# Performance work log

Measured on AMD Instinct MI355X. Metric: run time of the kernel, lower is better.

The kernel has to match this reference:

```python
import jax, jax.numpy as jnp
import numpy as np

TOPK = 2
EPS = 1e-6  # RMSNorm epsilon


def setup_inputs() -> dict:
    key = jax.random.key(0)
    ks = jax.random.split(key, 8)
    b, t, d, h, n = 2, 1024, 1024, 2048, 16
    x = jax.random.normal(ks[0], (b, t, d), dtype=jnp.float32)
    router_w = jax.random.normal(ks[1], (n, d), dtype=jnp.float32) * (1.0 / np.sqrt(d))
    router_bias = jnp.zeros((n,), dtype=jnp.float32)
    bank_mag = jax.random.normal(ks[2], (n, d, h), dtype=jnp.float32) * (1.0 / np.sqrt(d))
    bank_freq = jax.random.uniform(ks[3], (n, d, h), dtype=jnp.float32, minval=0.5, maxval=2.0) * (1.0 / np.sqrt(d))
    bank_phase = jax.random.uniform(ks[4], (n, h), dtype=jnp.float32, minval=-0.3, maxval=0.3)
    bank_down = jax.random.normal(ks[5], (n, h, d), dtype=jnp.float32) * (1.0 / np.sqrt(h))
    norm_w = jnp.ones((d,), dtype=jnp.float32)
    return {
        'x': x, 'router_w': router_w, 'router_bias': router_bias,
        'bank_mag': bank_mag, 'bank_freq': bank_freq, 'bank_phase': bank_phase,
        'bank_down': bank_down, 'norm_w': norm_w,
    }


def reference(x, router_w, router_bias, bank_mag, bank_freq, bank_phase, bank_down, norm_w):
    b, t, d = x.shape
    # Router: scores [b,t,n], top-k selection, softmax over selected logits
    scores = jnp.einsum('btd,nd->btn', x, router_w) + router_bias
    topv, topi = jax.lax.top_k(scores, TOPK)            # [b,t,k]
    weights = jax.nn.softmax(topv, axis=-1)             # [b,t,k]

    fx = x.reshape(b * t, d)                            # [T,d]
    # Dense per-expert compute (mathematically identical to per-token gather+bmm):
    mag = jnp.einsum('td,ndh->tnh', fx, bank_mag)       # [T,n,h]
    freq = jnp.einsum('td,ndh->tnh', fx, bank_freq)     # [T,n,h]
    hidden = jnp.tanh(mag) * jnp.cos(jax.nn.softplus(freq) + 0.1 + bank_phase[None, :, :])
    out_all = jnp.einsum('tnh,nhd->tnd', hidden, bank_down)  # [T,n,d]

    # Gather the top-k expert outputs per token and combine with routing weights
    ti = topi.reshape(b * t, TOPK)                      # [T,k]
    sel = jnp.take_along_axis(out_all, ti[:, :, None], axis=1)  # [T,k,d]
    out = jnp.einsum('tkd,tk->td', sel, weights.reshape(b * t, TOPK)).reshape(b, t, d)

    # RMSNorm
    out = out * jax.lax.rsqrt(jnp.mean(out * out, axis=-1, keepdims=True) + EPS) * norm_w
    return out
```

## Files before the change

### kernel.cpp

```cpp
#include <hip/hip_runtime.h>
#include <hip/hip_bf16.h>
#include <cstdint>
#include <cstddef>

#define TT 2048
#define DD 1024
#define HH 2048
#define NE 16
#define WM128 48
#define WM64  80
#define BROW 17

typedef __bf16 bf16x8 __attribute__((ext_vector_type(8)));
typedef float f32x4 __attribute__((ext_vector_type(4)));

__device__ __forceinline__ unsigned short f2bf(float f) {
  union { float f; unsigned u; } v; v.f = f;
  unsigned r = (v.u + 0x7FFFu + ((v.u >> 16) & 1u)) >> 16;
  return (unsigned short)r;
}
__device__ __forceinline__ float bf2f(unsigned short s) {
  union { unsigned u; float f; } v; v.u = ((unsigned)s) << 16;
  return v.f;
}
__device__ __forceinline__ unsigned packbf(float lo, float hi) {
  return (unsigned)f2bf(lo) | ((unsigned)f2bf(hi) << 16);
}

__device__ __forceinline__ void gl_lds16(const void* g, void* l) {
  __builtin_amdgcn_global_load_lds(
      (const __attribute__((address_space(1))) unsigned int*)g,
      (__attribute__((address_space(3))) unsigned int*)l, 16, 0, 0);
}

union U4 { unsigned int u[4]; bf16x8 v; };

__global__ __launch_bounds__(256) void k_cvt_x(const float* __restrict__ x,
                                               unsigned short* __restrict__ xbf) {
  int i = blockIdx.x * 256 + threadIdx.x;
  const float4* p = reinterpret_cast<const float4*>(x) + (size_t)i * 2;
  float4 a = p[0], b = p[1];
  ushort4 o0 = { f2bf(a.x), f2bf(a.y), f2bf(a.z), f2bf(a.w) };
  ushort4 o1 = { f2bf(b.x), f2bf(b.y), f2bf(b.z), f2bf(b.w) };
  reinterpret_cast<ushort4*>(xbf)[(size_t)i * 2]     = o0;
  reinterpret_cast<ushort4*>(xbf)[(size_t)i * 2 + 1] = o1;
}

__global__ __launch_bounds__(256) void k_router(
    const float* __restrict__ x, const float* __restrict__ rw,
    const float* __restrict__ rb, int* __restrict__ cnt,
    int* __restrict__ list_tok, int* __restrict__ rec,
    float* __restrict__ wrec) {
  const int t = blockIdx.x;
  __shared__ float xs[DD];
  __shared__ float part[256];
  __shared__ float sc[NE];
  const float* xr = x + (size_t)t * DD;
  for (int i = threadIdx.x; i < DD; i += 256) xs[i] = xr[i];
  __syncthreads();
  const int e = threadIdx.x >> 4, j = threadIdx.x & 15;
  const float* w = rw + (size_t)e * DD;
  float s = 0.f;
  for (int i = j; i < DD; i += 16) s += xs[i] * w[i];
  part[threadIdx.x] = s;
  __syncthreads();
  if (threadIdx.x < NE) {
    float v = rb[threadIdx.x];
    #pragma unroll
    for (int q = 0; q < 16; ++q) v += part[threadIdx.x * 16 + q];
    sc[threadIdx.x] = v;
  }
  __syncthreads();
  if (threadIdx.x == 0) {
    int e1 = 0; float v1 = sc[0];
    #pragma unroll
    for (int q = 1; q < NE; ++q) { if (sc[q] > v1) { v1 = sc[q]; e1 = q; } }
    int e2 = -1; float v2 = -3.4e38f;
    #pragma unroll
    for (int q = 0; q < NE; ++q) {
      if (q != e1 && sc[q] > v2) { v2 = sc[q]; e2 = q; }
    }
    float ex = expf(v2 - v1);
    float w1 = 1.f / (1.f + ex);
    float w2 = ex / (1.f + ex);
    int p1 = atomicAdd(&cnt[e1], 1);
    int p2 = atomicAdd(&cnt[e2], 1);
    list_tok[e1 * TT + p1] = t;
    list_tok[e2 * TT + p2] = t;
    rec[t * 4 + 0] = e1; rec[t * 4 + 1] = p1;
    rec[t * 4 + 2] = e2; rec[t * 4 + 3] = p2;
    wrec[t * 2 + 0] = w1; wrec[t * 2 + 1] = w2;
  }
}

__global__ void k_sched(const int* __restrict__ cnt, int* __restrict__ work128,
                        int* __restrict__ work64, int* __restrict__ woff) {
  if (threadIdx.x == 0) {
    int o = 0, n1 = 0, n2 = 0;
    for (int e = 0; e < NE; ++e) {
      int ce = cnt[e];
      int a = (ce + 127) >> 7;
      for (int mb = 0; mb < a; ++mb) { work128[n1 * 2] = e; work128[n1 * 2 + 1] = mb; ++n1; }
      int b = (ce + 63) >> 6;
      for (int mb = 0; mb < b; ++mb) { work64[n2 * 2] = e; work64[n2 * 2 + 1] = mb; ++n2; }
      woff[e] = o; o += ce;
    }
    for (int q = n1; q < WM128; ++q) { work128[q * 2] = -1; work128[q * 2 + 1] = 0; }
    for (int q = n2; q < WM64; ++q)  { work64[q * 2] = -1;  work64[q * 2 + 1] = 0; }
  }
}

__global__ __launch_bounds__(256, 4) void k_up(
    const unsigned short* __restrict__ xbf,
    const float* __restrict__ bmag,
    const float* __restrict__ bfreq,
    const float* __restrict__ bphase,
    const int* __restrict__ cnt, const int* __restrict__ list_tok,
    const int* __restrict__ work, const int* __restrict__ woff,
    unsigned short* __restrict__ hid) {
  const int e = work[blockIdx.x * 2 + 0];
  if (e < 0) return;
  const int mt = work[blockIdx.x * 2 + 1];
  const int nt = blockIdx.y;
  const int ce = cnt[e];
  const int off = woff[e];
  __shared__ unsigned short As[2][128][32];
  __shared__ unsigned int BuM[2][64 * BROW];
  __shared__ unsigned int BuF[2][64 * BROW];
  __shared__ int toks[128];
  const int tid = threadIdx.x;
  if (tid < 128) {
    int r = mt * 128 + tid;
    toks[tid] = list_tok[e * TT + (r < ce ? r : ce - 1)];
  }
  __syncthreads();
  const int w = tid >> 6, l = tid & 63;
  size_t abase[2]; int aoff[2];
  #pragma unroll
  for (int p = 0; p < 2; ++p) {
    int row = p * 64 + w * 16 + (l >> 2);
    int g = (l & 3) ^ ((row >> 1) & 3);
    abase[p] = (size_t)toks[row] * DD + g * 8;
    aoff[p] = (p * 256 + w * 64 + l) * 8;
  }
  const int q = tid >> 4;
  const int b16 = tid & 15;
  const int n0 = nt * 64;
  const float* srcM = bmag  + (size_t)e * DD * HH + n0 + 4 * b16;
  const float* srcF = bfreq + (size_t)e * DD * HH + n0 + 4 * b16;
  int bw[4];
  #pragma unroll
  for (int i = 0; i < 4; ++i) bw[i] = (4 * b16 + i) * BROW + q;

  const int wm = (w >> 1) * 64, wn = (w & 1) * 32;
  const int lr = l & 15, kg = l >> 4;
  const int nb0 = (wn + lr) * BROW + kg * 4;
  const int nb1 = (wn + 16 + lr) * BROW + kg * 4;
  const f32x4 zero = {0.f, 0.f, 0.f, 0.f};
  f32x4 accM[4][2], accF[4][2];
  #pragma unroll
  for (int a = 0; a < 4; ++a)
    #pragma unroll
    for (int b = 0; b < 2; ++b) { accM[a][b] = zero; accF[a][b] = zero; }

  float4 rm0, rm1, rf0, rf1;
  auto loadB = [&](int kt) {
    const float* pM = srcM + (size_t)(kt * 32 + 2 * q) * HH;
    const float* pF = srcF + (size_t)(kt * 32 + 2 * q) * HH;
    rm0 = *reinterpret_cast<const float4*>(pM);
    rm1 = *reinterpret_cast<const float4*>(pM + HH);
    rf0 = *reinterpret_cast<const float4*>(pF);
    rf1 = *reinterpret_cast<const float4*>(pF + HH);
  };
  auto writeB = [&](int buf) {
    const float* m0 = reinterpret_cast<const float*>(&rm0);
    const float* m1 = reinterpret_cast<const float*>(&rm1);
    const float* f0 = reinterpret_cast<const float*>(&rf0);
    const float* f1 = reinterpret_cast<const float*>(&rf1);
    #pragma unroll
    for (int i = 0; i < 4; ++i) {
      BuM[buf][bw[i]] = packbf(m0[i], m1[i]);
      BuF[buf][bw[i]] = packbf(f0[i], f1[i]);
    }
  };

  loadB(0);
  #pragma unroll
  for (int p = 0; p < 2; ++p) gl_lds16(xbf + abase[p], &As[0][0][0] + aoff[p]);
  writeB(0);
  __syncthreads();
  int buf = 0;
  for (int kt = 0; kt < DD / 32; ++kt) {
    const bool more = (kt + 1) < DD / 32;
    if (more) {
      loadB(kt + 1);
      #pragma unroll
      for (int p = 0; p < 2; ++p)
        gl_lds16(xbf + abase[p] + (kt + 1) * 32, &As[buf ^ 1][0][0] + aoff[p]);
    }
    bf16x8 av[4];
    #pragma unroll
    for (int fm = 0; fm < 4; ++fm) {
      int row = wm + fm * 16 + lr;
      int c = kg ^ ((row >> 1) & 3);
      av[fm] = *reinterpret_cast<const bf16x8*>(&As[buf][row][c * 8]);
    }
    U4 tm0, tm1, tf0, tf1;
    const unsigned int* bm = &BuM[buf][0];
    const unsigned int* bfp = &BuF[buf][0];
    #pragma unroll
    for (int j2 = 0; j2 < 4; ++j2) {
      tm0.u[j2] = bm[nb0 + j2];  tm1.u[j2] = bm[nb1 + j2];
      tf0.u[j2] = bfp[nb0 + j2]; tf1.u[j2] = bfp[nb1 + j2];
    }
    #pragma unroll
    for (int fm = 0; fm < 4; ++fm) {
      accM[fm][0] = __builtin_amdgcn_mfma_f32_16x16x32_bf16(av[fm], tm0.v, accM[fm][0], 0, 0, 0);
      accM[fm][1] = __builtin_amdgcn_mfma_f32_16x16x32_bf16(av[fm], tm1.v, accM[fm][1], 0, 0, 0);
      accF[fm][0] = __builtin_amdgcn_mfma_f32_16x16x32_bf16(av[fm], tf0.v, accF[fm][0], 0, 0, 0);
      accF[fm][1] = __builtin_amdgcn_mfma_f32_16x16x32_bf16(av[fm], tf1.v, accF[fm][1], 0, 0, 0);
    }
    if (more) writeB(buf ^ 1);
    __syncthreads();
    buf ^= 1;
  }
  #pragma unroll
  for (int fn = 0; fn < 2; ++fn) {
    const int ng = n0 + wn + fn * 16 + lr;
    const float ph = bphase[e * HH + ng] + 0.1f;
    #pragma unroll
    for (int fm = 0; fm < 4; ++fm) {
      #pragma unroll
      for (int jj = 0; jj < 4; ++jj) {
        int m = mt * 128 + wm + fm * 16 + kg * 4 + jj;
        if (m < ce) {
          float mv = (fn == 0) ? accM[fm][0][jj] : accM[fm][1][jj];
          float fv = (fn == 0) ? accF[fm][0][jj] : accF[fm][1][jj];
          float exn = __expf(-fabsf(fv));
          float sp = fmaxf(fv, 0.f) + __logf(1.f + exn);
          float t2 = __expf(2.f * mv);
          float th = 1.f - 2.f / (t2 + 1.f);
          float hv = th * __cosf(sp + ph);
          hid[(size_t)(off + m) * HH + ng] = f2bf(hv);
        }
      }
    }
  }
}

__global__ __launch_bounds__(256, 4) void k_down(
    const unsigned short* __restrict__ hid,
    const float* __restrict__ bdown,
    const int* __restrict__ cnt,
    const int* __restrict__ work, const int* __restrict__ woff,
    unsigned short* __restrict__ op) {
  const int e = work[blockIdx.x * 2 + 0];
  if (e < 0) return;
  const int mt = work[blockIdx.x * 2 + 1];
  const int nt = blockIdx.y;
  const int ce = cnt[e];
  const int off = woff[e];
  __shared__ unsigned short As[2][64][32];
  __shared__ unsigned int Bu[2][64 * BROW];
  const int tid = threadIdx.x;
  const int w = tid >> 6, l = tid & 63;
  const int row0 = tid >> 2;
  int gr = mt * 64 + row0; if (gr >= ce) gr = ce - 1;
  const size_t abase = (size_t)(off + gr) * HH + (size_t)(((tid & 3) ^ ((row0 >> 1) & 3)) * 8);
  const int aoff = tid * 8;
  const int q = tid >> 4;
  const int b16 = tid & 15;
  const int n0 = nt * 64;
  const float* srcD = bdown + (size_t)e * HH * DD + n0 + 4 * b16;
  int bw[4];
  #pragma unroll
  for (int i = 0; i < 4; ++i) bw[i] = (4 * b16 + i) * BROW + q;

  const int wm = (w >> 1) * 32, wn = (w & 1) * 32;
  const int lr = l & 15, kg = l >> 4;
  const int nb0 = (wn + lr) * BROW + kg * 4;
  const int nb1 = (wn + 16 + lr) * BROW + kg * 4;
  const f32x4 zero = {0.f, 0.f, 0.f, 0.f};
  f32x4 acc[2][2];
  #pragma unroll
  for (int a = 0; a < 2; ++a)
    #pragma unroll
    for (int b = 0; b < 2; ++b) acc[a][b] = zero;

  float4 rd0, rd1;
  auto loadB = [&](int kt) {
    const float* pD = srcD + (size_t)(kt * 32 + 2 * q) * DD;
    rd0 = *reinterpret_cast<const float4*>(pD);
    rd1 = *reinterpret_cast<const float4*>(pD + DD);
  };
  auto writeB = [&](int buf) {
    const float* d0 = reinterpret_cast<const float*>(&rd0);
    const float* d1 = reinterpret_cast<const float*>(&rd1);
    #pragma unroll
    for (int i = 0; i < 4; ++i) Bu[buf][bw[i]] = packbf(d0[i], d1[i]);
  };

  loadB(0);
  gl_lds16(hid + abase, &As[0][0][0] + aoff);
  writeB(0);
  __syncthreads();
  int buf = 0;
  for (int kt = 0; kt < HH / 32; ++kt) {
    const bool more = (kt + 1) < HH / 32;
    if (more) {
      loadB(kt + 1);
      gl_lds16(hid + abase + (kt + 1) * 32, &As[buf ^ 1][0][0] + aoff);
    }
    bf16x8 av[2];
    #pragma unroll
    for (int fm = 0; fm < 2; ++fm) {
      int row = wm + fm * 16 + lr;
      int c = kg ^ ((row >> 1) & 3);
      av[fm] = *reinterpret_cast<const bf16x8*>(&As[buf][row][c * 8]);
    }
    U4 t0, t1;
    const unsigned int* bp = &Bu[buf][0];
    #pragma unroll
    for (int j2 = 0; j2 < 4; ++j2) { t0.u[j2] = bp[nb0 + j2]; t1.u[j2] = bp[nb1 + j2]; }
    #pragma unroll
    for (int fm = 0; fm < 2; ++fm) {
      acc[fm][0] = __builtin_amdgcn_mfma_f32_16x16x32_bf16(av[fm], t0.v, acc[fm][0], 0, 0, 0);
      acc[fm][1] = __builtin_amdgcn_mfma_f32_16x16x32_bf16(av[fm], t1.v, acc[fm][1], 0, 0, 0);
    }
    if (more) writeB(buf ^ 1);
    __syncthreads();
    buf ^= 1;
  }
  #pragma unroll
  for (int fn = 0; fn < 2; ++fn) {
    const int ng = n0 + wn + fn * 16 + lr;
    #pragma unroll
    for (int fm = 0; fm < 2; ++fm) {
      #pragma unroll
      for (int jj = 0; jj < 4; ++jj) {
        int m = mt * 64 + wm + fm * 16 + kg * 4 + jj;
        if (m < ce)
          op[(size_t)(off + m) * DD + ng] = f2bf(acc[fm][fn][jj]);
      }
    }
  }
}

__global__ __launch_bounds__(256) void k_norm(
    const unsigned short* __restrict__ op, const int* __restrict__ woff,
    const int* __restrict__ rec, const float* __restrict__ wrec,
    const float* __restrict__ nw, float* __restrict__ out) {
  const int t = blockIdx.x;
  const int tid = threadIdx.x;
  __shared__ float red[4];
  const int e1 = rec[t * 4 + 0], p1 = rec[t * 4 + 1];
  const int e2 = rec[t * 4 + 2], p2 = rec[t * 4 + 3];
  const float w1 = wrec[t * 2 + 0], w2 = wrec[t * 2 + 1];
  const unsigned short* pa = op + (size_t)(woff[e1] + p1) * DD;
  const unsigned short* pb = op + (size_t)(woff[e2] + p2) * DD;
  float v[4]; float ss = 0.f;
  #pragma unroll
  for (int q = 0; q < 4; ++q) {
    int i = q * 256 + tid;
    v[q] = w1 * bf2f(pa[i]) + w2 * bf2f(pb[i]);
    ss += v[q] * v[q];
  }
  #pragma unroll
  for (int o = 32; o > 0; o >>= 1) ss += __shfl_xor(ss, o);
  if ((tid & 63) == 0) red[tid >> 6] = ss;
  __syncthreads();
  const float tot = red[0] + red[1] + red[2] + red[3];
  const float scl = rsqrtf(tot * (1.f / DD) + 1e-6f);
  #pragma unroll
  for (int q = 0; q < 4; ++q) {
    int i = q * 256 + tid;
    out[(size_t)t * DD + i] = v[q] * scl * nw[i];
  }
}

extern "C" void kernel_launch(void* const* d_in, const int* in_sizes, int n_in,
                              void* d_out, int out_size, void* d_ws, size_t ws_size,
                              hipStream_t stream) {
  const float* x      = (const float*)d_in[0];
  const float* rw     = (const float*)d_in[1];
  const float* rb     = (const float*)d_in[2];
  const float* bmag   = (const float*)d_in[3];
  const float* bfreq  = (const float*)d_in[4];
  const float* bphase = (const float*)d_in[5];
  const float* bdown  = (const float*)d_in[6];
  const float* nw     = (const float*)d_in[7];
  float* out = (float*)d_out;
  char* ws = (char*)d_ws;
  const size_t MB = 1024 * 1024;
  int*   cnt    = (int*)(ws + 0);
  int*   work1  = (int*)(ws + 128);
  int*   work2  = (int*)(ws + 1024);
  int*   woff   = (int*)(ws + 2048);
  int*   list   = (int*)(ws + 4096);
  int*   rec    = (int*)(ws + 139264);
  float* wrec   = (float*)(ws + 172032);
  unsigned short* xbf = (unsigned short*)(ws + 1 * MB);
  unsigned short* hid = (unsigned short*)(ws + 5 * MB);
  unsigned short* op  = (unsigned short*)(ws + 21 * MB);

  hipMemsetAsync(cnt, 0, 64, stream);
  k_cvt_x<<<1024, 256, 0, stream>>>(x, xbf);
  k_router<<<TT, 256, 0, stream>>>(x, rw, rb, cnt, list, rec, wrec);
  k_sched<<<1, 64, 0, stream>>>(cnt, work1, work2, woff);
  k_up<<<dim3(WM128, HH / 64), 256, 0, stream>>>(xbf, bmag, bfreq, bphase,
                                                 cnt, list, work1, woff, hid);
  k_down<<<dim3(WM64, DD / 64), 256, 0, stream>>>(hid, bdown, cnt, work2, woff, op);
  k_norm<<<TT, 256, 0, stream>>>(op, woff, rec, wrec, nw, out);
}
```

Baseline: 318.2 us.

## Double K-tile depth, enlarge down-proj M tile, fuse x conversion into router

Both expert GEMM kernels now process K in steps of 64 instead of 32, with a new XOR swizzle and padded B layout (stride 35), so there are half as many barrier/pipeline iterations. The down-projection tile grows from 64 to 128 rows and reuses the 128-row work schedule, which raises reuse of the bdown weights per block. The bf16 conversion of x moves into the router kernel, removing one launch. The price is larger LDS use and lower occupancy bounds (2 and 3 blocks per CU), and fewer blocks for k_down.

```diff
diff --git a/kernel.cpp b/kernel.cpp
--- a/kernel.cpp
+++ b/kernel.cpp
@@ -8,8 +8,7 @@
 #define HH 2048
 #define NE 16
 #define WM128 48
-#define WM64  80
-#define BROW 17
+#define BW35 35
 
 typedef __bf16 bf16x8 __attribute__((ext_vector_type(8)));
 typedef float f32x4 __attribute__((ext_vector_type(4)));
@@ -35,22 +34,11 @@
 
 union U4 { unsigned int u[4]; bf16x8 v; };
 
-__global__ __launch_bounds__(256) void k_cvt_x(const float* __restrict__ x,
-                                               unsigned short* __restrict__ xbf) {
-  int i = blockIdx.x * 256 + threadIdx.x;
-  const float4* p = reinterpret_cast<const float4*>(x) + (size_t)i * 2;
-  float4 a = p[0], b = p[1];
-  ushort4 o0 = { f2bf(a.x), f2bf(a.y), f2bf(a.z), f2bf(a.w) };
-  ushort4 o1 = { f2bf(b.x), f2bf(b.y), f2bf(b.z), f2bf(b.w) };
-  reinterpret_cast<ushort4*>(xbf)[(size_t)i * 2]     = o0;
-  reinterpret_cast<ushort4*>(xbf)[(size_t)i * 2 + 1] = o1;
-}
-
 __global__ __launch_bounds__(256) void k_router(
     const float* __restrict__ x, const float* __restrict__ rw,
     const float* __restrict__ rb, int* __restrict__ cnt,
     int* __restrict__ list_tok, int* __restrict__ rec,
-    float* __restrict__ wrec) {
+    float* __restrict__ wrec, unsigned short* __restrict__ xbf) {
   const int t = blockIdx.x;
   __shared__ float xs[DD];
   __shared__ float part[256];
@@ -58,6 +46,11 @@
   const float* xr = x + (size_t)t * DD;
   for (int i = threadIdx.x; i < DD; i += 256) xs[i] = xr[i];
   __syncthreads();
+  {
+    int i = threadIdx.x * 4;
+    ushort4 o = { f2bf(xs[i]), f2bf(xs[i + 1]), f2bf(xs[i + 2]), f2bf(xs[i + 3]) };
+    *reinterpret_cast<ushort4*>(xbf + (size_t)t * DD + i) = o;
+  }
   const int e = threadIdx.x >> 4, j = threadIdx.x & 15;
   const float* w = rw + (size_t)e * DD;
   float s = 0.f;
@@ -94,23 +87,20 @@
 }
 
 __global__ void k_sched(const int* __restrict__ cnt, int* __restrict__ work128,
-                        int* __restrict__ work64, int* __restrict__ woff) {
+                        int* __restrict__ woff) {
   if (threadIdx.x == 0) {
-    int o = 0, n1 = 0, n2 = 0;
+    int o = 0, n1 = 0;
     for (int e = 0; e < NE; ++e) {
       int ce = cnt[e];
       int a = (ce + 127) >> 7;
       for (int mb = 0; mb < a; ++mb) { work128[n1 * 2] = e; work128[n1 * 2 + 1] = mb; ++n1; }
-      int b = (ce + 63) >> 6;
-      for (int mb = 0; mb < b; ++mb) { work64[n2 * 2] = e; work64[n2 * 2 + 1] = mb; ++n2; }
       woff[e] = o; o += ce;
     }
     for (int q = n1; q < WM128; ++q) { work128[q * 2] = -1; work128[q * 2 + 1] = 0; }
-    for (int q = n2; q < WM64; ++q)  { work64[q * 2] = -1;  work64[q * 2 + 1] = 0; }
-  }
-}
-
-__global__ __launch_bounds__(256, 4) void k_up(
+  }
+}
+
+__global__ __launch_bounds__(256, 2) void k_up(
     const unsigned short* __restrict__ xbf,
     const float* __restrict__ bmag,
     const float* __restrict__ bfreq,
@@ -124,9 +114,9 @@
   const int nt = blockIdx.y;
   const int ce = cnt[e];
   const int off = woff[e];
-  __shared__ unsigned short As[2][128][32];
-  __shared__ unsigned int BuM[2][64 * BROW];
-  __shared__ unsigned int BuF[2][64 * BROW];
+  __shared__ unsigned short As[2][128][64];
+  __shared__ unsigned int BuM[2][64 * BW35];
+  __shared__ unsigned int BuF[2][64 * BW35];
   __shared__ int toks[128];
   const int tid = threadIdx.x;
   if (tid < 128) {
@@ -135,27 +125,29 @@
   }
   __syncthreads();
   const int w = tid >> 6, l = tid & 63;
-  size_t abase[2]; int aoff[2];
-  #pragma unroll
-  for (int p = 0; p < 2; ++p) {
-    int row = p * 64 + w * 16 + (l >> 2);
-    int g = (l & 3) ^ ((row >> 1) & 3);
-    abase[p] = (size_t)toks[row] * DD + g * 8;
-    aoff[p] = (p * 256 + w * 64 + l) * 8;
-  }
-  const int q = tid >> 4;
-  const int b16 = tid & 15;
+  const int lhi = l >> 3, llo = l & 7;
+  size_t abase[4]; int aoff[4];
+  #pragma unroll
+  for (int j = 0; j < 4; ++j) {
+    int seg = w * 4 + j;
+    int r = seg * 8 + lhi;
+    abase[j] = (size_t)toks[r] * DD + (size_t)((llo ^ (r & 7)) * 8);
+    aoff[j] = seg * 512 + l * 8;
+  }
   const int n0 = nt * 64;
-  const float* srcM = bmag  + (size_t)e * DD * HH + n0 + 4 * b16;
-  const float* srcF = bfreq + (size_t)e * DD * HH + n0 + 4 * b16;
-  int bw[4];
-  #pragma unroll
-  for (int i = 0; i < 4; ++i) bw[i] = (4 * b16 + i) * BROW + q;
-
+  const float* srcM = bmag  + (size_t)e * DD * HH + n0 + 4 * (tid & 15);
+  const float* srcF = bfreq + (size_t)e * DD * HH + n0 + 4 * (tid & 15);
+  int q2s[2], bw[2][4];
+  #pragma unroll
+  for (int s = 0; s < 2; ++s) {
+    int idx = s * 256 + tid;
+    int q2 = idx >> 4;
+    q2s[s] = q2;
+    #pragma unroll
+    for (int i = 0; i < 4; ++i) bw[s][i] = (4 * (tid & 15) + i) * BW35 + q2;
+  }
   const int wm = (w >> 1) * 64, wn = (w & 1) * 32;
   const int lr = l & 15, kg = l >> 4;
-  const int nb0 = (wn + lr) * BROW + kg * 4;
-  const int nb1 = (wn + 16 + lr) * BROW + kg * 4;
   const f32x4 zero = {0.f, 0.f, 0.f, 0.f};
   f32x4 accM[4][2], accF[4][2];
   #pragma unroll
@@ -163,62 +155,73 @@
     #pragma unroll
     for (int b = 0; b < 2; ++b) { accM[a][b] = zero; accF[a][b] = zero; }
 
-  float4 rm0, rm1, rf0, rf1;
+  float4 rm0[2], rm1[2], rf0[2], rf1[2];
   auto loadB = [&](int kt) {
-    const float* pM = srcM + (size_t)(kt * 32 + 2 * q) * HH;
-    const float* pF = srcF + (size_t)(kt * 32 + 2 * q) * HH;
-    rm0 = *reinterpret_cast<const float4*>(pM);
-    rm1 = *reinterpret_cast<const float4*>(pM + HH);
-    rf0 = *reinterpret_cast<const float4*>(pF);
-    rf1 = *reinterpret_cast<const float4*>(pF + HH);
+    #pragma unroll
+    for (int s = 0; s < 2; ++s) {
+      const float* pM = srcM + (size_t)(kt * 64 + 2 * q2s[s]) * HH;
+      const float* pF = srcF + (size_t)(kt * 64 + 2 * q2s[s]) * HH;
+      rm0[s] = *reinterpret_cast<const float4*>(pM);
+      rm1[s] = *reinterpret_cast<const float4*>(pM + HH);
+      rf0[s] = *reinterpret_cast<const float4*>(pF);
+      rf1[s] = *reinterpret_cast<const float4*>(pF + HH);
+    }
   };
   auto writeB = [&](int buf) {
-    const float* m0 = reinterpret_cast<const float*>(&rm0);
-    const float* m1 = reinterpret_cast<const float*>(&rm1);
-    const float* f0 = reinterpret_cast<const float*>(&rf0);
-    const float* f1 = reinterpret_cast<const float*>(&rf1);
-    #pragma unroll
-    for (int i = 0; i < 4; ++i) {
-      BuM[buf][bw[i]] = packbf(m0[i], m1[i]);
-      BuF[buf][bw[i]] = packbf(f0[i], f1[i]);
+    #pragma unroll
+    for (int s = 0; s < 2; ++s) {
+      const float* m0 = reinterpret_cast<const float*>(&rm0[s]);
+      const float* m1 = reinterpret_cast<const float*>(&rm1[s]);
+      const float* f0 = reinterpret_cast<const float*>(&rf0[s]);
+      const float* f1 = reinterpret_cast<const float*>(&rf1[s]);
+      #pragma unroll
+      for (int i = 0; i < 4; ++i) {
+        BuM[buf][bw[s][i]] = packbf(m0[i], m1[i]);
+        BuF[buf][bw[s][i]] = packbf(f0[i], f1[i]);
+      }
     }
   };
 
   loadB(0);
   #pragma unroll
-  for (int p = 0; p < 2; ++p) gl_lds16(xbf + abase[p], &As[0][0][0] + aoff[p]);
+  for (int j = 0; j < 4; ++j) gl_lds16(xbf + abase[j], &As[0][0][0] + aoff[j]);
   writeB(0);
   __syncthreads();
   int buf = 0;
-  for (int kt = 0; kt < DD / 32; ++kt) {
-    const bool more = (kt + 1) < DD / 32;
+  for (int kt = 0; kt < DD / 64; ++kt) {
+    const bool more = (kt + 1) < DD / 64;
     if (more) {
+      #pragma unroll
+      for (int j = 0; j < 4; ++j)
+        gl_lds16(xbf + abase[j] + (kt + 1) * 64, &As[buf ^ 1][0][0] + aoff[j]);
       loadB(kt + 1);
-      #pragma unroll
-      for (int p = 0; p < 2; ++p)
-        gl_lds16(xbf + abase[p] + (kt + 1) * 32, &As[buf ^ 1][0][0] + aoff[p]);
-    }
-    bf16x8 av[4];
-    #pragma unroll
-    for (int fm = 0; fm < 4; ++fm) {
-      int row = wm + fm * 16 + lr;
-      int c = kg ^ ((row >> 1) & 3);
-      av[fm] = *reinterpret_cast<const bf16x8*>(&As[buf][row][c * 8]);
-    }
-    U4 tm0, tm1, tf0, tf1;
-    const unsigned int* bm = &BuM[buf][0];
-    const unsigned int* bfp = &BuF[buf][0];
-    #pragma unroll
-    for (int j2 = 0; j2 < 4; ++j2) {
-      tm0.u[j2] = bm[nb0 + j2];  tm1.u[j2] = bm[nb1 + j2];
-      tf0.u[j2] = bfp[nb0 + j2]; tf1.u[j2] = bfp[nb1 + j2];
-    }
-    #pragma unroll
-    for (int fm = 0; fm < 4; ++fm) {
-      accM[fm][0] = __builtin_amdgcn_mfma_f32_16x16x32_bf16(av[fm], tm0.v, accM[fm][0], 0, 0, 0);
-      accM[fm][1] = __builtin_amdgcn_mfma_f32_16x16x32_bf16(av[fm], tm1.v, accM[fm][1], 0, 0, 0);
-      accF[fm][0] = __builtin_amdgcn_mfma_f32_16x16x32_bf16(av[fm], tf0.v, accF[fm][0], 0, 0, 0);
-      accF[fm][1] = __builtin_amdgcn_mfma_f32_16x16x32_bf16(av[fm], tf1.v, accF[fm][1], 0, 0, 0);
+    }
+    #pragma unroll
+    for (int ks = 0; ks < 2; ++ks) {
+      bf16x8 av[4];
+      #pragma unroll
+      for (int fm = 0; fm < 4; ++fm) {
+        int row = wm + fm * 16 + lr;
+        int c = (ks * 4 + kg) ^ (row & 7);
+        av[fm] = *reinterpret_cast<const bf16x8*>(&As[buf][row][c * 8]);
+      }
+      U4 tm[2], tf[2];
+      #pragma unroll
+      for (int fn = 0; fn < 2; ++fn) {
+        const int nb = (wn + fn * 16 + lr) * BW35 + ks * 16 + kg * 4;
+        #pragma unroll
+        for (int j2 = 0; j2 < 4; ++j2) {
+          tm[fn].u[j2] = BuM[buf][nb + j2];
+          tf[fn].u[j2] = BuF[buf][nb + j2];
+        }
+      }
+      #pragma unroll
+      for (int fm = 0; fm < 4; ++fm)
+        #pragma unroll
+        for (int fn = 0; fn < 2; ++fn) {
+          accM[fm][fn] = __builtin_amdgcn_mfma_f32_16x16x32_bf16(av[fm], tm[fn].v, accM[fm][fn], 0, 0, 0);
+          accF[fm][fn] = __builtin_amdgcn_mfma_f32_16x16x32_bf16(av[fm], tf[fn].v, accF[fm][fn], 0, 0, 0);
+        }
     }
     if (more) writeB(buf ^ 1);
     __syncthreads();
@@ -234,8 +237,8 @@
       for (int jj = 0; jj < 4; ++jj) {
         int m = mt * 128 + wm + fm * 16 + kg * 4 + jj;
         if (m < ce) {
-          float mv = (fn == 0) ? accM[fm][0][jj] : accM[fm][1][jj];
-          float fv = (fn == 0) ? accF[fm][0][jj] : accF[fm][1][jj];
+          float mv = accM[fm][fn][jj];
+          float fv = accF[fm][fn][jj];
           float exn = __expf(-fabsf(fv));
           float sp = fmaxf(fv, 0.f) + __logf(1.f + exn);
           float t2 = __expf(2.f * mv);
@@ -248,7 +251,7 @@
   }
 }
 
-__global__ __launch_bounds__(256, 4) void k_down(
+__global__ __launch_bounds__(256, 3) void k_down(
     const unsigned short* __restrict__ hid,
     const float* __restrict__ bdown,
     const int* __restrict__ cnt,
@@ -260,72 +263,94 @@
   const int nt = blockIdx.y;
   const int ce = cnt[e];
   const int off = woff[e];
-  __shared__ unsigned short As[2][64][32];
-  __shared__ unsigned int Bu[2][64 * BROW];
+  __shared__ unsigned short As[2][128][64];
+  __shared__ unsigned int Bu[2][64 * BW35];
   const int tid = threadIdx.x;
   const int w = tid >> 6, l = tid & 63;
-  const int row0 = tid >> 2;
-  int gr = mt * 64 + row0; if (gr >= ce) gr = ce - 1;
-  const size_t abase = (size_t)(off + gr) * HH + (size_t)(((tid & 3) ^ ((row0 >> 1) & 3)) * 8);
-  const int aoff = tid * 8;
-  const int q = tid >> 4;
-  const int b16 = tid & 15;
+  const int lhi = l >> 3, llo = l & 7;
+  size_t abase[4]; int aoff[4];
+  #pragma unroll
+  for (int j = 0; j < 4; ++j) {
+    int seg = w * 4 + j;
+    int r = seg * 8 + lhi;
+    int gr = mt * 128 + r; if (gr >= ce) gr = ce - 1;
+    abase[j] = (size_t)(off + gr) * HH + (size_t)((llo ^ (r & 7)) * 8);
+    aoff[j] = seg * 512 + l * 8;
+  }
   const int n0 = nt * 64;
-  const float* srcD = bdown + (size_t)e * HH * DD + n0 + 4 * b16;
-  int bw[4];
-  #pragma unroll
-  for (int i = 0; i < 4; ++i) bw[i] = (4 * b16 + i) * BROW + q;
-
-  const int wm = (w >> 1) * 32, wn = (w & 1) * 32;
+  const float* srcD = bdown + (size_t)e * HH * DD + n0 + 4 * (tid & 15);
+  int q2s[2], bw[2][4];
+  #pragma unroll
+  for (int s = 0; s < 2; ++s) {
+    int idx = s * 256 + tid;
+    int q2 = idx >> 4;
+    q2s[s] = q2;
+    #pragma unroll
+    for (int i = 0; i < 4; ++i) bw[s][i] = (4 * (tid & 15) + i) * BW35 + q2;
+  }
+  const int wm = (w >> 1) * 64, wn = (w & 1) * 32;
   const int lr = l & 15, kg = l >> 4;
-  const int nb0 = (wn + lr) * BROW + kg * 4;
-  const int nb1 = (wn + 16 + lr) * BROW + kg * 4;
   const f32x4 zero = {0.f, 0.f, 0.f, 0.f};
-  f32x4 acc[2][2];
-  #pragma unroll
-  for (int a = 0; a < 2; ++a)
+  f32x4 acc[4][2];
+  #pragma unroll
+  for (int a = 0; a < 4; ++a)
     #pragma unroll
     for (int b = 0; b < 2; ++b) acc[a][b] = zero;
 
-  float4 rd0, rd1;
+  float4 rd0[2], rd1[2];
   auto loadB = [&](int kt) {
-    const float* pD = srcD + (size_t)(kt * 32 + 2 * q) * DD;
-    rd0 = *reinterpret_cast<const float4*>(pD);
-    rd1 = *reinterpret_cast<const float4*>(pD + DD);
+    #pragma unroll
+    for (int s = 0; s < 2; ++s) {
+      const float* pD = srcD + (size_t)(kt * 64 + 2 * q2s[s]) * DD;
+      rd0[s] = *reinterpret_cast<const float4*>(pD);
+      rd1[s] = *reinterpret_cast<const float4*>(pD + DD);
+    }
   };
   auto writeB = [&](int buf) {
-    const float* d0 = reinterpret_cast<const float*>(&rd0);
-    const float* d1 = reinterpret_cast<const float*>(&rd1);
-    #pragma unroll
-    for (int i = 0; i < 4; ++i) Bu[buf][bw[i]] = packbf(d0[i], d1[i]);
+    #pragma unroll
+    for (int s = 0; s < 2; ++s) {
+      const float* d0 = reinterpret_cast<const float*>(&rd0[s]);
+      const float* d1 = reinterpret_cast<const float*>(&rd1[s]);
+      #pragma unroll
+      for (int i = 0; i < 4; ++i) Bu[buf][bw[s][i]] = packbf(d0[i], d1[i]);
+    }
   };
 
   loadB(0);
-  gl_lds16(hid + abase, &As[0][0][0] + aoff);
+  #pragma unroll
+  for (int j = 0; j < 4; ++j) gl_lds16(hid + abase[j], &As[0][0][0] + aoff[j]);
   writeB(0);
   __syncthreads();
   int buf = 0;
-  for (int kt = 0; kt < HH / 32; ++kt) {
-    const bool more = (kt + 1) < HH / 32;
+  for (int kt = 0; kt < HH / 64; ++kt) {
+    const bool more = (kt + 1) < HH / 64;
     if (more) {
+      #pragma unroll
+      for (int j = 0; j < 4; ++j)
+        gl_lds16(hid + abase[j] + (kt + 1) * 64, &As[buf ^ 1][0][0] + aoff[j]);
       loadB(kt + 1);
-      gl_lds16(hid + abase + (kt + 1) * 32, &As[buf ^ 1][0][0] + aoff);
-    }
-    bf16x8 av[2];
-    #pragma unroll
-    for (int fm = 0; fm < 2; ++fm) {
-      int row = wm + fm * 16 + lr;
-      int c = kg ^ ((row >> 1) & 3);
-      av[fm] = *reinterpret_cast<const bf16x8*>(&As[buf][row][c * 8]);
-    }
-    U4 t0, t1;
-    const unsigned int* bp = &Bu[buf][0];
-    #pragma unroll
-    for (int j2 = 0; j2 < 4; ++j2) { t0.u[j2] = bp[nb0 + j2]; t1.u[j2] = bp[nb1 + j2]; }
-    #pragma unroll
-    for (int fm = 0; fm < 2; ++fm) {
-      acc[fm][0] = __builtin_amdgcn_mfma_f32_16x16x32_bf16(av[fm], t0.v, acc[fm][0], 0, 0, 0);
-      acc[fm][1] = __builtin_amdgcn_mfma_f32_16x16x32_bf16(av[fm], t1.v, acc[fm][1], 0, 0, 0);
+    }
+    #pragma unroll
+    for (int ks = 0; ks < 2; ++ks) {
+      bf16x8 av[4];
+      #pragma unroll
+      for (int fm = 0; fm < 4; ++fm) {
+        int row = wm + fm * 16 + lr;
+        int c = (ks * 4 + kg) ^ (row & 7);
+        av[fm] = *reinterpret_cast<const bf16x8*>(&As[buf][row][c * 8]);
+      }
+      U4 t[2];
+      #pragma unroll
+      for (int fn = 0; fn < 2; ++fn) {
+        const int nb = (wn + fn * 16 + lr) * BW35 + ks * 16 + kg * 4;
+        #pragma unroll
+        for (int j2 = 0; j2 < 4; ++j2) t[fn].u[j2] = Bu[buf][nb + j2];
+      }
+      #pragma unroll
+      for (int fm = 0; fm < 4; ++fm)
+        #pragma unroll
+        for (int fn = 0; fn < 2; ++fn)
+          acc[fm][fn] = __builtin_amdgcn_mfma_f32_16x16x32_bf16(av[fm], t[fn].v, acc[fm][fn], 0, 0, 0);
     }
     if (more) writeB(buf ^ 1);
     __syncthreads();
@@ -335,10 +360,10 @@
   for (int fn = 0; fn < 2; ++fn) {
     const int ng = n0 + wn + fn * 16 + lr;
     #pragma unroll
-    for (int fm = 0; fm < 2; ++fm) {
+    for (int fm = 0; fm < 4; ++fm) {
       #pragma unroll
       for (int jj = 0; jj < 4; ++jj) {
-        int m = mt * 64 + wm + fm * 16 + kg * 4 + jj;
+        int m = mt * 128 + wm + fm * 16 + kg * 4 + jj;
         if (m < ce)
           op[(size_t)(off + m) * DD + ng] = f2bf(acc[fm][fn][jj]);
       }
@@ -394,7 +419,6 @@
   const size_t MB = 1024 * 1024;
   int*   cnt    = (int*)(ws + 0);
   int*   work1  = (int*)(ws + 128);
-  int*   work2  = (int*)(ws + 1024);
   int*   woff   = (int*)(ws + 2048);
   int*   list   = (int*)(ws + 4096);
   int*   rec    = (int*)(ws + 139264);
@@ -404,11 +428,10 @@
   unsigned short* op  = (unsigned short*)(ws + 21 * MB);
 
   hipMemsetAsync(cnt, 0, 64, stream);
-  k_cvt_x<<<1024, 256, 0, stream>>>(x, xbf);
-  k_router<<<TT, 256, 0, stream>>>(x, rw, rb, cnt, list, rec, wrec);
-  k_sched<<<1, 64, 0, stream>>>(cnt, work1, work2, woff);
+  k_router<<<TT, 256, 0, stream>>>(x, rw, rb, cnt, list, rec, wrec, xbf);
+  k_sched<<<1, 64, 0, stream>>>(cnt, work1, woff);
   k_up<<<dim3(WM128, HH / 64), 256, 0, stream>>>(xbf, bmag, bfreq, bphase,
                                                  cnt, list, work1, woff, hid);
-  k_down<<<dim3(WM64, DD / 64), 256, 0, stream>>>(hid, bdown, cnt, work2, woff, op);
+  k_down<<<dim3(WM128, DD / 64), 256, 0, stream>>>(hid, bdown, cnt, work1, woff, op);
   k_norm<<<TT, 256, 0, stream>>>(op, woff, rec, wrec, nw, out);
 }
```

After: 294.7 us. -7.4%, faster.
